# Kernel optimization log

Measured on AMD Instinct MI355X. Metric: run time of the kernel, lower is better.

The kernel has to match this reference:

```python
import jax, jax.numpy as jnp
import numpy as np

N_Q = 16384; N_S = 16384; NN = 32; F_IN = 128; F_OUT = 256
K = 15; DIM = 3
RADIUS = 10.0
KP_EXTENT_CFG = 1.0      # config.NETWORK.KP_EXTENT (also scales learned offsets)
DENSITY = 5.0            # config.NETWORK.DENSITY_PARAMETER
EXTENT = KP_EXTENT_CFG * RADIUS / DENSITY   # 2.0
K_RADIUS = 1.5 * EXTENT
OFFSET_DIM = DIM * (K - 1)  # modulated=False, version=0 -> 42


def setup_inputs() -> dict:
    key = jax.random.key(0)
    ks = jax.random.split(key, 8)
    query_points = jax.random.uniform(ks[0], (N_Q, DIM), dtype=jnp.float32)
    support_points = jax.random.uniform(ks[1], (N_S, DIM), dtype=jnp.float32)
    neighbors = jax.random.randint(ks[2], (N_Q, NN), 0, N_S)
    features = jax.random.normal(ks[3], (N_S, F_IN), dtype=jnp.float32)
    # kernel points: fixed disposition inside ball of radius 1.5*extent, first point at center
    kp = jax.random.normal(ks[4], (K, DIM), dtype=jnp.float32)
    kp = kp / jnp.linalg.norm(kp, axis=1, keepdims=True) * (0.7 * K_RADIUS)
    K_points = kp.at[0].set(0.0)
    weight = jax.random.normal(ks[5], (K, F_IN, F_OUT), dtype=jnp.float32) / np.sqrt(F_IN)
    deformable_weight = jax.random.normal(ks[6], (K, F_IN, OFFSET_DIM), dtype=jnp.float32) / np.sqrt(F_IN)
    bias = jnp.zeros((OFFSET_DIM,), dtype=jnp.float32)
    return {"query_points": query_points, "support_points": support_points,
            "neighbors": neighbors, "features": features, "K_points": K_points,
            "weight": weight, "deformable_weight": deformable_weight, "bias": bias}


def _gather_neighb(query_points, support_points, neighbors, features):
    # pad with shadow point (far away) and zero feature row, as in KPConv_ops
    sp = jnp.concatenate([support_points, jnp.full((1, DIM), 1e6, support_points.dtype)], 0)
    ft = jnp.concatenate([features, jnp.zeros((1, features.shape[1]), features.dtype)], 0)
    rel = sp[neighbors] - query_points[:, None, :]   # [n, nn, 3]
    nfeat = ft[neighbors]                            # [n, nn, f]
    return rel, nfeat


def _linear_influence(sq_dist):
    # KP_INFLUENCE='linear': relu(1 - d/extent); CONVOLUTION_MODE='sum'
    return jnp.maximum(1.0 - jnp.sqrt(sq_dist) / EXTENT, 0.0)


def reference(query_points, support_points, neighbors, features, K_points,
              weight, deformable_weight, bias):
    rel, nfeat = _gather_neighb(query_points, support_points, neighbors, features)

    # --- rigid KPConv producing offsets (version=0) ---
    d0 = rel[:, :, None, :] - K_points[None, None, :, :]   # [n, nn, K, 3]
    sq0 = jnp.sum(d0 * d0, axis=-1)                        # [n, nn, K]
    w0 = _linear_influence(sq0)
    wf0 = jnp.einsum('enk,enf->ekf', w0, nfeat)            # [n, K, f]
    feat0 = jnp.einsum('ekf,kfo->eo', wf0, deformable_weight) + bias  # [n, 42]

    # not modulated: reshape to offsets, prepend zero offset for center kernel point
    offsets = feat0.reshape(-1, K - 1, DIM)
    offsets = jnp.concatenate([jnp.zeros_like(offsets[:, :1, :]), offsets], axis=1)
    offsets = offsets * KP_EXTENT_CFG                      # [n, K, 3]

    # --- deformable KPConv ---
    def_kp = K_points[None, :, :] + offsets                # [n, K, 3]
    d1 = rel[:, :, None, :] - def_kp[:, None, :, :]        # [n, nn, K, 3]
    sq1 = jnp.sum(d1 * d1, axis=-1)                        # [n, nn, K]
    w1 = _linear_influence(sq1)                            # out-of-range neighbors get 0 weight
    wf1 = jnp.einsum('enk,enf->ekf', w1, nfeat)            # [n, K, f]
    out = jnp.einsum('ekf,kfo->eo', wf1, weight)           # [n, f_out]
    return out
```

## Files before the change

### kernel.cpp

```cpp
#include <hip/hip_runtime.h>
#include <hip/hip_bf16.h>
#include <math.h>

typedef __attribute__((ext_vector_type(8))) short bf16x8;
typedef __attribute__((ext_vector_type(4))) float f32x4;

#define NQ 16384
#define NN 32
#define FI 128
#define FO 256
#define KPN 15
#define OD 42
#define INV_EXT 0.5f

#define WS_FP1    0u
#define WS_FP2    (8u * 1024u * 1024u)
#define WS_BSW    (12u * 1024u * 1024u)
#define WS_DWBH   (13u * 1024u * 1024u)
#define WS_DWBL   (WS_DWBH + 196608u)
#define WS_DEFKP  (14u * 1024u * 1024u)

static __device__ __forceinline__ unsigned short f2bf(float x) {
    union { __hip_bfloat16 h; unsigned short u; } cv;
    cv.h = __float2bfloat16(x);
    return cv.u;
}
static __device__ __forceinline__ float bf2f(unsigned short h) {
    union { unsigned int u; float f; } cv;
    cv.u = ((unsigned int)h) << 16;
    return cv.f;
}

union U8 { unsigned short u[8]; bf16x8 v; };

__global__ void pre_all(const float* __restrict__ feat,
                        unsigned int* __restrict__ fp1, unsigned int* __restrict__ fp2,
                        const float* __restrict__ w, unsigned short* __restrict__ Bsw,
                        const float* __restrict__ dw,
                        unsigned short* __restrict__ dhi, unsigned short* __restrict__ dlo)
{
    const int b = blockIdx.x, t = threadIdx.x;
    if (b < 4096) {
        const int tid = b * 256 + t;
        const int s = tid >> 6, r = tid & 63;
        const int fp = r >> 4, low = r & 15;
        const float a = feat[s * FI + fp * 32 + low];
        const float c = feat[s * FI + fp * 32 + 16 + low];
        const unsigned short ha = f2bf(a), hc = f2bf(c);
        const unsigned int w0 = (unsigned int)ha | ((unsigned int)hc << 16);
        const unsigned int w1 = (unsigned int)f2bf(a - bf2f(ha)) |
                                ((unsigned int)f2bf(c - bf2f(hc)) << 16);
        uint2 pr; pr.x = w0; pr.y = w1;
        *(uint2*)&fp1[s * 128 + fp * 32 + low * 2] = pr;
        fp2[s * 64 + fp * 16 + low] = w0;
    } else if (b < 4096 + 256) {
        const int tid = (b - 4096) * 256 + t;
        const int lane = tid & 63;
        const int kt   = (tid >> 6) & 63;
        const int nt   = tid >> 12;
        const int n    = nt * 16 + (lane & 15);
        const int kbase = kt * 32 + (lane >> 4) * 8;
        unsigned int p[4];
        #pragma unroll
        for (int jj = 0; jj < 4; jj++) {
            unsigned int lo, hi;
            {
                const int kk = kbase + 2 * jj;
                const int f = kk >> 4, k = kk & 15;
                lo = (k < KPN) ? f2bf(w[(k * FI + f) * FO + n]) : 0u;
            }
            {
                const int kk = kbase + 2 * jj + 1;
                const int f = kk >> 4, k = kk & 15;
                hi = (k < KPN) ? f2bf(w[(k * FI + f) * FO + n]) : 0u;
            }
            p[jj] = lo | (hi << 16);
        }
        unsigned int* op = (unsigned int*)&Bsw[tid * 8];
        op[0] = p[0]; op[1] = p[1]; op[2] = p[2]; op[3] = p[3];
    } else {
        const int tid = (b - 4352) * 256 + t;
        const int lane = tid & 63;
        const int kt   = (tid >> 6) & 63;
        const int nt   = tid >> 12;
        const int o    = nt * 16 + (lane & 15);
        const int kbase = kt * 32 + (lane >> 4) * 8;
        #pragma unroll
        for (int j = 0; j < 8; j++) {
            const int kf = kbase + j;
            const int f = kf >> 4, k = kf & 15;
            float v = (k < KPN && o < OD) ? dw[(k * FI + f) * OD + o] : 0.f;
            unsigned short h = f2bf(v);
            dhi[tid * 8 + j] = h;
            dlo[tid * 8 + j] = f2bf(v - bf2f(h));
        }
    }
}

__global__ __launch_bounds__(512, 4)
void k1_offsets(const float* __restrict__ query, const float* __restrict__ support,
                const int* __restrict__ neighbors, const unsigned int* __restrict__ fp1,
                const float* __restrict__ kpoints,
                const unsigned short* __restrict__ dwB_hi,
                const unsigned short* __restrict__ dwB_lo,
                const float* __restrict__ bias, float* __restrict__ defkp)
{
    __shared__ unsigned short wfA_hi[8192];
    __shared__ unsigned short wfA_lo[8192];
    __shared__ float relx[512], rely[512], relz[512];
    __shared__ int   nbr_s[512];
    __shared__ float kp_s[48];
    __shared__ f32x4 cred[3 * 64];

    const int t = threadIdx.x;
    const int qbase = blockIdx.x * 16;
    if (t < 45) kp_s[t] = kpoints[t];
    if (t >= 45 && t < 48) kp_s[t] = 0.f;

    {
        const int e = t >> 5, n = t & 31;
        const int q = qbase + e;
        const int idx = neighbors[q * NN + n];
        nbr_s[t] = idx;
        relx[t] = support[idx * 3 + 0] - query[q * 3 + 0];
        rely[t] = support[idx * 3 + 1] - query[q * 3 + 1];
        relz[t] = support[idx * 3 + 2] - query[q * 3 + 2];
    }
    __syncthreads();

    const int wave = t >> 6, lane = t & 63;
    const int quad = lane >> 4, low = lane & 15;
    const int ee0 = wave * 2;

    const int kb = (low < KPN) ? low * 3 : 0;
    const float kx = kp_s[kb + 0], ky = kp_s[kb + 1], kz = kp_s[kb + 2];
    U8 ah[2], al[2];
    #pragma unroll
    for (int ei = 0; ei < 2; ei++) {
        #pragma unroll
        for (int j = 0; j < 8; j++) {
            const int ni = (ee0 + ei) * 32 + quad * 8 + j;
            const float dx = relx[ni] - kx;
            const float dy = rely[ni] - ky;
            const float dz = relz[ni] - kz;
            const float d = sqrtf(dx * dx + dy * dy + dz * dz);
            float w = 1.0f - d * INV_EXT;
            w = (low < KPN && w > 0.f) ? w : 0.f;
            const unsigned short h = f2bf(w);
            ah[ei].u[j] = h;
            al[ei].u[j] = f2bf(w - bf2f(h));
        }
    }

    f32x4 acc = {0.f, 0.f, 0.f, 0.f};
    const int nt = wave >> 1, half = wave & 1;

    for (int c = 0; c < 4; c++) {
        #pragma unroll
        for (int ei = 0; ei < 2; ei++) {
            const int ee = ee0 + ei;
            union { unsigned int u[4]; bf16x8 v; } bhA, blA, bhB, blB;
            #pragma unroll
            for (int jj = 0; jj < 4; jj++) {
                const int r0 = nbr_s[ee * 32 + quad * 8 + 2 * jj];
                const int r1 = nbr_s[ee * 32 + quad * 8 + 2 * jj + 1];
                const uint2 d0 = *(const uint2*)&fp1[r0 * 128 + c * 32 + low * 2];
                const uint2 d1 = *(const uint2*)&fp1[r1 * 128 + c * 32 + low * 2];
                bhA.u[jj] = __builtin_amdgcn_perm(d1.x, d0.x, 0x05040100u);
                bhB.u[jj] = __builtin_amdgcn_perm(d1.x, d0.x, 0x07060302u);
                blA.u[jj] = __builtin_amdgcn_perm(d1.y, d0.y, 0x05040100u);
                blB.u[jj] = __builtin_amdgcn_perm(d1.y, d0.y, 0x07060302u);
            }
            #pragma unroll
            for (int hh2 = 0; hh2 < 2; hh2++) {
                const bf16x8 bh = hh2 ? bhB.v : bhA.v;
                const bf16x8 bl = hh2 ? blB.v : blA.v;
                f32x4 o = {0.f, 0.f, 0.f, 0.f};
                o = __builtin_amdgcn_mfma_f32_16x16x32_bf16(al[ei].v, bh, o, 0, 0, 0);
                o = __builtin_amdgcn_mfma_f32_16x16x32_bf16(ah[ei].v, bl, o, 0, 0, 0);
                o = __builtin_amdgcn_mfma_f32_16x16x32_bf16(ah[ei].v, bh, o, 0, 0, 0);
                const int cblk = (hh2 * 16 + low) * 2 + (quad >> 1);
                const int hw = cblk * 128 + ((ee ^ (cblk & 15)) * 8) + (quad & 1) * 4;
                const unsigned short h0 = f2bf(o[0]), h1 = f2bf(o[1]);
                const unsigned short h2 = f2bf(o[2]), h3 = f2bf(o[3]);
                uint2 ph;
                ph.x = (unsigned int)h0 | ((unsigned int)h1 << 16);
                ph.y = (unsigned int)h2 | ((unsigned int)h3 << 16);
                *(uint2*)&wfA_hi[hw] = ph;
                uint2 pl;
                pl.x = (unsigned int)f2bf(o[0] - bf2f(h0)) |
                       ((unsigned int)f2bf(o[1] - bf2f(h1)) << 16);
                pl.y = (unsigned int)f2bf(o[2] - bf2f(h2)) |
                       ((unsigned int)f2bf(o[3] - bf2f(h3)) << 16);
                *(uint2*)&wfA_lo[hw] = pl;
            }
        }
        __syncthreads();
        if (wave < 6) {
            const bf16x8* Bh = (const bf16x8*)dwB_hi;
            const bf16x8* Bl = (const bf16x8*)dwB_lo;
            #pragma unroll 4
            for (int ktl = half * 8; ktl < half * 8 + 8; ktl++) {
                const int cblk = ktl * 4 + quad;
                const int hw = cblk * 128 + ((low ^ (cblk & 15)) * 8);
                bf16x8 a_h = *(const bf16x8*)&wfA_hi[hw];
                bf16x8 a_l = *(const bf16x8*)&wfA_lo[hw];
                const int ktg = c * 16 + ktl;
                bf16x8 b_h = Bh[(nt * 64 + ktg) * 64 + lane];
                bf16x8 b_l = Bl[(nt * 64 + ktg) * 64 + lane];
                acc = __builtin_amdgcn_mfma_f32_16x16x32_bf16(a_l, b_h, acc, 0, 0, 0);
                acc = __builtin_amdgcn_mfma_f32_16x16x32_bf16(a_h, b_l, acc, 0, 0, 0);
                acc = __builtin_amdgcn_mfma_f32_16x16x32_bf16(a_h, b_h, acc, 0, 0, 0);
            }
        } else if (c == 0 && wave == 6 && lane < 48) {
            defkp[(qbase + lane / 3) * 45 + (lane % 3)] = kp_s[lane % 3];
        }
        __syncthreads();
    }

    if (wave < 6 && half == 1) cred[nt * 64 + lane] = acc;
    __syncthreads();
    if (wave < 6 && half == 0) {
        f32x4 o2 = cred[nt * 64 + lane];
        acc[0] += o2[0]; acc[1] += o2[1]; acc[2] += o2[2]; acc[3] += o2[3];
        const int o = nt * 16 + low;
        if (o < OD) {
            const float bo = bias[o] + kp_s[3 + o];
            #pragma unroll
            for (int r = 0; r < 4; r++) {
                const int ee = quad * 4 + r;
                defkp[(qbase + ee) * 45 + 3 + o] = bo + acc[r];
            }
        }
    }
}

__global__ __launch_bounds__(512, 4)
void k2_deform(const float* __restrict__ query, const float* __restrict__ support,
               const int* __restrict__ neighbors, const unsigned int* __restrict__ fp2,
               const unsigned short* __restrict__ Bsw, const float* __restrict__ defkp,
               float* __restrict__ out)
{
    __shared__ unsigned short wfA[16384];
    __shared__ float relx[1024], rely[1024], relz[1024];
    __shared__ float dk_s[32 * 45];
    __shared__ unsigned short nbr_s[1024];

    const int t = threadIdx.x;
    const int qbase = blockIdx.x * 32;

    for (int i = t; i < 32 * 45; i += 512) dk_s[i] = defkp[qbase * 45 + i];
    #pragma unroll
    for (int ii = 0; ii < 2; ii++) {
        const int i = ii * 512 + t;
        const int e = i >> 5, n = i & 31;
        const int q = qbase + e;
        const int idx = neighbors[q * NN + n];
        nbr_s[i] = (unsigned short)idx;
        relx[i] = support[idx * 3 + 0] - query[q * 3 + 0];
        rely[i] = support[idx * 3 + 1] - query[q * 3 + 1];
        relz[i] = support[idx * 3 + 2] - query[q * 3 + 2];
    }
    __syncthreads();

    const int wave = t >> 6, lane = t & 63;
    const int quad = lane >> 4, low = lane & 15;
    const int ee0 = wave * 4;
    const int kb = (low < KPN) ? low * 3 : 0;

    U8 af[4];
    #pragma unroll
    for (int ei = 0; ei < 4; ei++) {
        const int ee = ee0 + ei;
        const float kx = dk_s[ee * 45 + kb + 0];
        const float ky = dk_s[ee * 45 + kb + 1];
        const float kz = dk_s[ee * 45 + kb + 2];
        #pragma unroll
        for (int j = 0; j < 8; j++) {
            const int ni = ee * 32 + quad * 8 + j;
            const float dx = relx[ni] - kx;
            const float dy = rely[ni] - ky;
            const float dz = relz[ni] - kz;
            const float d = sqrtf(dx * dx + dy * dy + dz * dz);
            float w = 1.0f - d * INV_EXT;
            w = (low < KPN && w > 0.f) ? w : 0.f;
            af[ei].u[j] = f2bf(w);
        }
    }

    f32x4 acc00 = {0,0,0,0}, acc01 = {0,0,0,0};
    f32x4 acc10 = {0,0,0,0}, acc11 = {0,0,0,0};
    const int nt0 = wave * 2, nt1 = nt0 + 1;
    const bf16x8* Bp = (const bf16x8*)Bsw;

    for (int c = 0; c < 4; c++) {
        #pragma unroll
        for (int ei = 0; ei < 4; ei++) {
            const int ee = ee0 + ei;
            union { unsigned int u[4]; bf16x8 v; } bA, bB;
            #pragma unroll
            for (int jj = 0; jj < 4; jj++) {
                const int r0 = nbr_s[ee * 32 + quad * 8 + 2 * jj];
                const int r1 = nbr_s[ee * 32 + quad * 8 + 2 * jj + 1];
                const unsigned int d0 = fp2[r0 * 64 + c * 16 + low];
                const unsigned int d1 = fp2[r1 * 64 + c * 16 + low];
                bA.u[jj] = __builtin_amdgcn_perm(d1, d0, 0x05040100u);
                bB.u[jj] = __builtin_amdgcn_perm(d1, d0, 0x07060302u);
            }
            #pragma unroll
            for (int hh2 = 0; hh2 < 2; hh2++) {
                const bf16x8 b = hh2 ? bB.v : bA.v;
                f32x4 o = {0.f, 0.f, 0.f, 0.f};
                o = __builtin_amdgcn_mfma_f32_16x16x32_bf16(af[ei].v, b, o, 0, 0, 0);
                const int cblk = (hh2 * 16 + low) * 2 + (quad >> 1);
                const int hw = cblk * 256 + ((ee ^ (cblk & 31)) * 8) + (quad & 1) * 4;
                uint2 ph;
                ph.x = (unsigned int)f2bf(o[0]) | ((unsigned int)f2bf(o[1]) << 16);
                ph.y = (unsigned int)f2bf(o[2]) | ((unsigned int)f2bf(o[3]) << 16);
                *(uint2*)&wfA[hw] = ph;
            }
        }
        __syncthreads();
        #pragma unroll 4
        for (int ktl = 0; ktl < 16; ktl++) {
            const int cblk = ktl * 4 + quad;
            const int s0 = (low ^ (cblk & 31)) * 8;
            const int s1 = ((16 + low) ^ (cblk & 31)) * 8;
            bf16x8 a0 = *(const bf16x8*)&wfA[cblk * 256 + s0];
            bf16x8 a1 = *(const bf16x8*)&wfA[cblk * 256 + s1];
            const int ktg = c * 16 + ktl;
            bf16x8 b0 = Bp[(nt0 * 64 + ktg) * 64 + lane];
            bf16x8 b1 = Bp[(nt1 * 64 + ktg) * 64 + lane];
            acc00 = __builtin_amdgcn_mfma_f32_16x16x32_bf16(a0, b0, acc00, 0, 0, 0);
            acc01 = __builtin_amdgcn_mfma_f32_16x16x32_bf16(a0, b1, acc01, 0, 0, 0);
            acc10 = __builtin_amdgcn_mfma_f32_16x16x32_bf16(a1, b0, acc10, 0, 0, 0);
            acc11 = __builtin_amdgcn_mfma_f32_16x16x32_bf16(a1, b1, acc11, 0, 0, 0);
        }
        __syncthreads();
    }

    #pragma unroll
    for (int r = 0; r < 4; r++) {
        const int e0 = quad * 4 + r;
        out[(qbase + e0) * FO + nt0 * 16 + low] = acc00[r];
        out[(qbase + e0) * FO + nt1 * 16 + low] = acc01[r];
        out[(qbase + 16 + e0) * FO + nt0 * 16 + low] = acc10[r];
        out[(qbase + 16 + e0) * FO + nt1 * 16 + low] = acc11[r];
    }
}

extern "C" void kernel_launch(void* const* d_in, const int* in_sizes, int n_in,
                              void* d_out, int out_size, void* d_ws, size_t ws_size,
                              hipStream_t stream) {
    const float* query     = (const float*)d_in[0];
    const float* support   = (const float*)d_in[1];
    const int*   neighbors = (const int*)  d_in[2];
    const float* features  = (const float*)d_in[3];
    const float* kpoints   = (const float*)d_in[4];
    const float* weight    = (const float*)d_in[5];
    const float* dweight   = (const float*)d_in[6];
    const float* bias      = (const float*)d_in[7];
    float*       out       = (float*)d_out;

    char* ws = (char*)d_ws;
    unsigned int*   fp1  = (unsigned int*)(ws + WS_FP1);
    unsigned int*   fp2  = (unsigned int*)(ws + WS_FP2);
    unsigned short* Bsw  = (unsigned short*)(ws + WS_BSW);
    unsigned short* dwBh = (unsigned short*)(ws + WS_DWBH);
    unsigned short* dwBl = (unsigned short*)(ws + WS_DWBL);
    float*          defkp = (float*)(ws + WS_DEFKP);

    pre_all<<<4400, 256, 0, stream>>>(features, fp1, fp2, weight, Bsw,
                                      dweight, dwBh, dwBl);
    k1_offsets<<<NQ / 16, 512, 0, stream>>>(query, support, neighbors, fp1,
                                            kpoints, dwBh, dwBl, bias, defkp);
    k2_deform<<<NQ / 32, 512, 0, stream>>>(query, support, neighbors, fp2,
                                           Bsw, defkp, out);
}
```

Baseline: 167.7 us.

## Fuse offset KPConv and deformable KPConv into one kernel per 32 queries

Merges the offset-producing kernel and the deformable convolution kernel into a single kernel handling 32 queries per block. The deformed kernel points stay in shared memory instead of going through a global buffer, and the neighbor and relative-position setup is shared between both stages. The offset GEMM is re-tiled so that 6 waves each cover one of 3 output tiles for one of two 16-query halves, which removes the cross-wave reduction. The cost is higher shared memory per block (two 32 KB feature tiles plus position arrays), which may lower occupancy, and half as many blocks for the offset stage.

```diff
diff --git a/kernel.cpp b/kernel.cpp
--- a/kernel.cpp
+++ b/kernel.cpp
@@ -18,7 +18,6 @@
 #define WS_BSW    (12u * 1024u * 1024u)
 #define WS_DWBH   (13u * 1024u * 1024u)
 #define WS_DWBL   (WS_DWBH + 196608u)
-#define WS_DEFKP  (14u * 1024u * 1024u)
 
 static __device__ __forceinline__ unsigned short f2bf(float x) {
     union { __hip_bfloat16 h; unsigned short u; } cv;
@@ -98,158 +97,25 @@
 }
 
 __global__ __launch_bounds__(512, 4)
-void k1_offsets(const float* __restrict__ query, const float* __restrict__ support,
-                const int* __restrict__ neighbors, const unsigned int* __restrict__ fp1,
-                const float* __restrict__ kpoints,
-                const unsigned short* __restrict__ dwB_hi,
-                const unsigned short* __restrict__ dwB_lo,
-                const float* __restrict__ bias, float* __restrict__ defkp)
+void k_fused(const float* __restrict__ query, const float* __restrict__ support,
+             const int* __restrict__ neighbors, const unsigned int* __restrict__ fp1,
+             const unsigned int* __restrict__ fp2, const float* __restrict__ kpoints,
+             const unsigned short* __restrict__ dwB_hi,
+             const unsigned short* __restrict__ dwB_lo,
+             const unsigned short* __restrict__ Bsw,
+             const float* __restrict__ bias, float* __restrict__ out)
 {
-    __shared__ unsigned short wfA_hi[8192];
-    __shared__ unsigned short wfA_lo[8192];
-    __shared__ float relx[512], rely[512], relz[512];
-    __shared__ int   nbr_s[512];
+    __shared__ unsigned short wf_hi[16384];
+    __shared__ unsigned short wf_lo[16384];
+    __shared__ float relx[1024], rely[1024], relz[1024];
+    __shared__ unsigned short nbr_s[1024];
     __shared__ float kp_s[48];
-    __shared__ f32x4 cred[3 * 64];
 
     const int t = threadIdx.x;
-    const int qbase = blockIdx.x * 16;
+    const int qbase = blockIdx.x * 32;
     if (t < 45) kp_s[t] = kpoints[t];
     if (t >= 45 && t < 48) kp_s[t] = 0.f;
 
-    {
-        const int e = t >> 5, n = t & 31;
-        const int q = qbase + e;
-        const int idx = neighbors[q * NN + n];
-        nbr_s[t] = idx;
-        relx[t] = support[idx * 3 + 0] - query[q * 3 + 0];
-        rely[t] = support[idx * 3 + 1] - query[q * 3 + 1];
-        relz[t] = support[idx * 3 + 2] - query[q * 3 + 2];
-    }
-    __syncthreads();
-
-    const int wave = t >> 6, lane = t & 63;
-    const int quad = lane >> 4, low = lane & 15;
-    const int ee0 = wave * 2;
-
-    const int kb = (low < KPN) ? low * 3 : 0;
-    const float kx = kp_s[kb + 0], ky = kp_s[kb + 1], kz = kp_s[kb + 2];
-    U8 ah[2], al[2];
-    #pragma unroll
-    for (int ei = 0; ei < 2; ei++) {
-        #pragma unroll
-        for (int j = 0; j < 8; j++) {
-            const int ni = (ee0 + ei) * 32 + quad * 8 + j;
-            const float dx = relx[ni] - kx;
-            const float dy = rely[ni] - ky;
-            const float dz = relz[ni] - kz;
-            const float d = sqrtf(dx * dx + dy * dy + dz * dz);
-            float w = 1.0f - d * INV_EXT;
-            w = (low < KPN && w > 0.f) ? w : 0.f;
-            const unsigned short h = f2bf(w);
-            ah[ei].u[j] = h;
-            al[ei].u[j] = f2bf(w - bf2f(h));
-        }
-    }
-
-    f32x4 acc = {0.f, 0.f, 0.f, 0.f};
-    const int nt = wave >> 1, half = wave & 1;
-
-    for (int c = 0; c < 4; c++) {
-        #pragma unroll
-        for (int ei = 0; ei < 2; ei++) {
-            const int ee = ee0 + ei;
-            union { unsigned int u[4]; bf16x8 v; } bhA, blA, bhB, blB;
-            #pragma unroll
-            for (int jj = 0; jj < 4; jj++) {
-                const int r0 = nbr_s[ee * 32 + quad * 8 + 2 * jj];
-                const int r1 = nbr_s[ee * 32 + quad * 8 + 2 * jj + 1];
-                const uint2 d0 = *(const uint2*)&fp1[r0 * 128 + c * 32 + low * 2];
-                const uint2 d1 = *(const uint2*)&fp1[r1 * 128 + c * 32 + low * 2];
-                bhA.u[jj] = __builtin_amdgcn_perm(d1.x, d0.x, 0x05040100u);
-                bhB.u[jj] = __builtin_amdgcn_perm(d1.x, d0.x, 0x07060302u);
-                blA.u[jj] = __builtin_amdgcn_perm(d1.y, d0.y, 0x05040100u);
-                blB.u[jj] = __builtin_amdgcn_perm(d1.y, d0.y, 0x07060302u);
-            }
-            #pragma unroll
-            for (int hh2 = 0; hh2 < 2; hh2++) {
-                const bf16x8 bh = hh2 ? bhB.v : bhA.v;
-                const bf16x8 bl = hh2 ? blB.v : blA.v;
-                f32x4 o = {0.f, 0.f, 0.f, 0.f};
-                o = __builtin_amdgcn_mfma_f32_16x16x32_bf16(al[ei].v, bh, o, 0, 0, 0);
-                o = __builtin_amdgcn_mfma_f32_16x16x32_bf16(ah[ei].v, bl, o, 0, 0, 0);
-                o = __builtin_amdgcn_mfma_f32_16x16x32_bf16(ah[ei].v, bh, o, 0, 0, 0);
-                const int cblk = (hh2 * 16 + low) * 2 + (quad >> 1);
-                const int hw = cblk * 128 + ((ee ^ (cblk & 15)) * 8) + (quad & 1) * 4;
-                const unsigned short h0 = f2bf(o[0]), h1 = f2bf(o[1]);
-                const unsigned short h2 = f2bf(o[2]), h3 = f2bf(o[3]);
-                uint2 ph;
-                ph.x = (unsigned int)h0 | ((unsigned int)h1 << 16);
-                ph.y = (unsigned int)h2 | ((unsigned int)h3 << 16);
-                *(uint2*)&wfA_hi[hw] = ph;
-                uint2 pl;
-                pl.x = (unsigned int)f2bf(o[0] - bf2f(h0)) |
-                       ((unsigned int)f2bf(o[1] - bf2f(h1)) << 16);
-                pl.y = (unsigned int)f2bf(o[2] - bf2f(h2)) |
-                       ((unsigned int)f2bf(o[3] - bf2f(h3)) << 16);
-                *(uint2*)&wfA_lo[hw] = pl;
-            }
-        }
-        __syncthreads();
-        if (wave < 6) {
-            const bf16x8* Bh = (const bf16x8*)dwB_hi;
-            const bf16x8* Bl = (const bf16x8*)dwB_lo;
-            #pragma unroll 4
-            for (int ktl = half * 8; ktl < half * 8 + 8; ktl++) {
-                const int cblk = ktl * 4 + quad;
-                const int hw = cblk * 128 + ((low ^ (cblk & 15)) * 8);
-                bf16x8 a_h = *(const bf16x8*)&wfA_hi[hw];
-                bf16x8 a_l = *(const bf16x8*)&wfA_lo[hw];
-                const int ktg = c * 16 + ktl;
-                bf16x8 b_h = Bh[(nt * 64 + ktg) * 64 + lane];
-                bf16x8 b_l = Bl[(nt * 64 + ktg) * 64 + lane];
-                acc = __builtin_amdgcn_mfma_f32_16x16x32_bf16(a_l, b_h, acc, 0, 0, 0);
-                acc = __builtin_amdgcn_mfma_f32_16x16x32_bf16(a_h, b_l, acc, 0, 0, 0);
-                acc = __builtin_amdgcn_mfma_f32_16x16x32_bf16(a_h, b_h, acc, 0, 0, 0);
-            }
-        } else if (c == 0 && wave == 6 && lane < 48) {
-            defkp[(qbase + lane / 3) * 45 + (lane % 3)] = kp_s[lane % 3];
-        }
-        __syncthreads();
-    }
-
-    if (wave < 6 && half == 1) cred[nt * 64 + lane] = acc;
-    __syncthreads();
-    if (wave < 6 && half == 0) {
-        f32x4 o2 = cred[nt * 64 + lane];
-        acc[0] += o2[0]; acc[1] += o2[1]; acc[2] += o2[2]; acc[3] += o2[3];
-        const int o = nt * 16 + low;
-        if (o < OD) {
-            const float bo = bias[o] + kp_s[3 + o];
-            #pragma unroll
-            for (int r = 0; r < 4; r++) {
-                const int ee = quad * 4 + r;
-                defkp[(qbase + ee) * 45 + 3 + o] = bo + acc[r];
-            }
-        }
-    }
-}
-
-__global__ __launch_bounds__(512, 4)
-void k2_deform(const float* __restrict__ query, const float* __restrict__ support,
-               const int* __restrict__ neighbors, const unsigned int* __restrict__ fp2,
-               const unsigned short* __restrict__ Bsw, const float* __restrict__ defkp,
-               float* __restrict__ out)
-{
-    __shared__ unsigned short wfA[16384];
-    __shared__ float relx[1024], rely[1024], relz[1024];
-    __shared__ float dk_s[32 * 45];
-    __shared__ unsigned short nbr_s[1024];
-
-    const int t = threadIdx.x;
-    const int qbase = blockIdx.x * 32;
-
-    for (int i = t; i < 32 * 45; i += 512) dk_s[i] = defkp[qbase * 45 + i];
     #pragma unroll
     for (int ii = 0; ii < 2; ii++) {
         const int i = ii * 512 + t;
@@ -265,16 +131,122 @@
 
     const int wave = t >> 6, lane = t & 63;
     const int quad = lane >> 4, low = lane & 15;
-    const int ee0 = wave * 4;
     const int kb = (low < KPN) ? low * 3 : 0;
+
+    U8 ah[4], al[4];
+    {
+        const float kx = kp_s[kb + 0], ky = kp_s[kb + 1], kz = kp_s[kb + 2];
+        #pragma unroll
+        for (int ei = 0; ei < 4; ei++) {
+            const int ee = wave * 4 + ei;
+            #pragma unroll
+            for (int j = 0; j < 8; j++) {
+                const int ni = ee * 32 + quad * 8 + j;
+                const float dx = relx[ni] - kx;
+                const float dy = rely[ni] - ky;
+                const float dz = relz[ni] - kz;
+                const float d = sqrtf(dx * dx + dy * dy + dz * dz);
+                float w = 1.0f - d * INV_EXT;
+                w = (low < KPN && w > 0.f) ? w : 0.f;
+                const unsigned short h = f2bf(w);
+                ah[ei].u[j] = h;
+                al[ei].u[j] = f2bf(w - bf2f(h));
+            }
+        }
+    }
+
+    f32x4 acc = {0.f, 0.f, 0.f, 0.f};
+    const int et = (wave >= 3) ? 1 : 0;
+    const int nt = wave - et * 3;
+
+    for (int c = 0; c < 4; c++) {
+        #pragma unroll 2
+        for (int ei = 0; ei < 4; ei++) {
+            const int ee = wave * 4 + ei;
+            union { unsigned int u[4]; bf16x8 v; } bhA, blA, bhB, blB;
+            #pragma unroll
+            for (int jj = 0; jj < 4; jj++) {
+                const int r0 = nbr_s[ee * 32 + quad * 8 + 2 * jj];
+                const int r1 = nbr_s[ee * 32 + quad * 8 + 2 * jj + 1];
+                const uint2 d0 = *(const uint2*)&fp1[r0 * 128 + c * 32 + low * 2];
+                const uint2 d1 = *(const uint2*)&fp1[r1 * 128 + c * 32 + low * 2];
+                bhA.u[jj] = __builtin_amdgcn_perm(d1.x, d0.x, 0x05040100u);
+                bhB.u[jj] = __builtin_amdgcn_perm(d1.x, d0.x, 0x07060302u);
+                blA.u[jj] = __builtin_amdgcn_perm(d1.y, d0.y, 0x05040100u);
+                blB.u[jj] = __builtin_amdgcn_perm(d1.y, d0.y, 0x07060302u);
+            }
+            #pragma unroll
+            for (int hh2 = 0; hh2 < 2; hh2++) {
+                const bf16x8 bh = hh2 ? bhB.v : bhA.v;
+                const bf16x8 bl = hh2 ? blB.v : blA.v;
+                f32x4 o = {0.f, 0.f, 0.f, 0.f};
+                o = __builtin_amdgcn_mfma_f32_16x16x32_bf16(al[ei].v, bh, o, 0, 0, 0);
+                o = __builtin_amdgcn_mfma_f32_16x16x32_bf16(ah[ei].v, bl, o, 0, 0, 0);
+                o = __builtin_amdgcn_mfma_f32_16x16x32_bf16(ah[ei].v, bh, o, 0, 0, 0);
+                const int fc   = hh2 * 16 + low;
+                const int cblk = fc + (quad >> 1) * 32;
+                const int slot = ee ^ fc;
+                const int hw   = cblk * 256 + slot * 8 + (quad & 1) * 4;
+                const unsigned short h0 = f2bf(o[0]), h1 = f2bf(o[1]);
+                const unsigned short h2 = f2bf(o[2]), h3 = f2bf(o[3]);
+                uint2 ph;
+                ph.x = (unsigned int)h0 | ((unsigned int)h1 << 16);
+                ph.y = (unsigned int)h2 | ((unsigned int)h3 << 16);
+                *(uint2*)&wf_hi[hw] = ph;
+                uint2 pl;
+                pl.x = (unsigned int)f2bf(o[0] - bf2f(h0)) |
+                       ((unsigned int)f2bf(o[1] - bf2f(h1)) << 16);
+                pl.y = (unsigned int)f2bf(o[2] - bf2f(h2)) |
+                       ((unsigned int)f2bf(o[3] - bf2f(h3)) << 16);
+                *(uint2*)&wf_lo[hw] = pl;
+            }
+        }
+        __syncthreads();
+        if (wave < 6) {
+            const bf16x8* Bh = (const bf16x8*)dwB_hi;
+            const bf16x8* Bl = (const bf16x8*)dwB_lo;
+            #pragma unroll 4
+            for (int ktl = 0; ktl < 16; ktl++) {
+                const int fcq  = ktl * 2 + (quad >> 1);
+                const int cblk = fcq + (quad & 1) * 32;
+                const int slot = (et * 16 + low) ^ fcq;
+                bf16x8 a_h = *(const bf16x8*)&wf_hi[cblk * 256 + slot * 8];
+                bf16x8 a_l = *(const bf16x8*)&wf_lo[cblk * 256 + slot * 8];
+                const int ktg = c * 16 + ktl;
+                bf16x8 b_h = Bh[(nt * 64 + ktg) * 64 + lane];
+                bf16x8 b_l = Bl[(nt * 64 + ktg) * 64 + lane];
+                acc = __builtin_amdgcn_mfma_f32_16x16x32_bf16(a_l, b_h, acc, 0, 0, 0);
+                acc = __builtin_amdgcn_mfma_f32_16x16x32_bf16(a_h, b_l, acc, 0, 0, 0);
+                acc = __builtin_amdgcn_mfma_f32_16x16x32_bf16(a_h, b_h, acc, 0, 0, 0);
+            }
+        }
+        __syncthreads();
+    }
+
+    float* dk_s = (float*)wf_lo;
+    if (wave < 6) {
+        const int o = nt * 16 + low;
+        if (o < OD) {
+            const float bo = bias[o] + kp_s[3 + o];
+            #pragma unroll
+            for (int r = 0; r < 4; r++) {
+                const int ee = et * 16 + quad * 4 + r;
+                dk_s[ee * 48 + 3 + o] = bo + acc[r];
+            }
+        }
+    } else {
+        const int idx2 = (wave - 6) * 64 + lane;
+        if (idx2 < 96) dk_s[(idx2 / 3) * 48 + (idx2 % 3)] = kp_s[idx2 % 3];
+    }
+    __syncthreads();
 
     U8 af[4];
     #pragma unroll
     for (int ei = 0; ei < 4; ei++) {
-        const int ee = ee0 + ei;
-        const float kx = dk_s[ee * 45 + kb + 0];
-        const float ky = dk_s[ee * 45 + kb + 1];
-        const float kz = dk_s[ee * 45 + kb + 2];
+        const int ee = wave * 4 + ei;
+        const float kx = dk_s[ee * 48 + kb + 0];
+        const float ky = dk_s[ee * 48 + kb + 1];
+        const float kz = dk_s[ee * 48 + kb + 2];
         #pragma unroll
         for (int j = 0; j < 8; j++) {
             const int ni = ee * 32 + quad * 8 + j;
@@ -296,7 +268,7 @@
     for (int c = 0; c < 4; c++) {
         #pragma unroll
         for (int ei = 0; ei < 4; ei++) {
-            const int ee = ee0 + ei;
+            const int ee = wave * 4 + ei;
             union { unsigned int u[4]; bf16x8 v; } bA, bB;
             #pragma unroll
             for (int jj = 0; jj < 4; jj++) {
@@ -312,22 +284,25 @@
                 const bf16x8 b = hh2 ? bB.v : bA.v;
                 f32x4 o = {0.f, 0.f, 0.f, 0.f};
                 o = __builtin_amdgcn_mfma_f32_16x16x32_bf16(af[ei].v, b, o, 0, 0, 0);
-                const int cblk = (hh2 * 16 + low) * 2 + (quad >> 1);
-                const int hw = cblk * 256 + ((ee ^ (cblk & 31)) * 8) + (quad & 1) * 4;
+                const int fc   = hh2 * 16 + low;
+                const int cblk = fc + (quad >> 1) * 32;
+                const int slot = ee ^ fc;
+                const int hw   = cblk * 256 + slot * 8 + (quad & 1) * 4;
                 uint2 ph;
                 ph.x = (unsigned int)f2bf(o[0]) | ((unsigned int)f2bf(o[1]) << 16);
                 ph.y = (unsigned int)f2bf(o[2]) | ((unsigned int)f2bf(o[3]) << 16);
-                *(uint2*)&wfA[hw] = ph;
+                *(uint2*)&wf_hi[hw] = ph;
             }
         }
         __syncthreads();
         #pragma unroll 4
         for (int ktl = 0; ktl < 16; ktl++) {
-            const int cblk = ktl * 4 + quad;
-            const int s0 = (low ^ (cblk & 31)) * 8;
-            const int s1 = ((16 + low) ^ (cblk & 31)) * 8;
-            bf16x8 a0 = *(const bf16x8*)&wfA[cblk * 256 + s0];
-            bf16x8 a1 = *(const bf16x8*)&wfA[cblk * 256 + s1];
+            const int fcq  = ktl * 2 + (quad >> 1);
+            const int cblk = fcq + (quad & 1) * 32;
+            const int s0 = (low ^ fcq) * 8;
+            const int s1 = ((16 + low) ^ fcq) * 8;
+            bf16x8 a0 = *(const bf16x8*)&wf_hi[cblk * 256 + s0];
+            bf16x8 a1 = *(const bf16x8*)&wf_hi[cblk * 256 + s1];
             const int ktg = c * 16 + ktl;
             bf16x8 b0 = Bp[(nt0 * 64 + ktg) * 64 + lane];
             bf16x8 b1 = Bp[(nt1 * 64 + ktg) * 64 + lane];
@@ -368,12 +343,9 @@
     unsigned short* Bsw  = (unsigned short*)(ws + WS_BSW);
     unsigned short* dwBh = (unsigned short*)(ws + WS_DWBH);
     unsigned short* dwBl = (unsigned short*)(ws + WS_DWBL);
-    float*          defkp = (float*)(ws + WS_DEFKP);
 
     pre_all<<<4400, 256, 0, stream>>>(features, fp1, fp2, weight, Bsw,
                                       dweight, dwBh, dwBl);
-    k1_offsets<<<NQ / 16, 512, 0, stream>>>(query, support, neighbors, fp1,
-                                            kpoints, dwBh, dwBl, bias, defkp);
-    k2_deform<<<NQ / 32, 512, 0, stream>>>(query, support, neighbors, fp2,
-                                           Bsw, defkp, out);
-}
+    k_fused<<<NQ / 32, 512, 0, stream>>>(query, support, neighbors, fp1, fp2,
+                                         kpoints, dwBh, dwBl, Bsw, bias, out);
+}
```

Result: slower. 178.6 us (+6.5%).

## Vectorize feature packing and widen k2 gathers to two feature chunks per pass

Applied to the files above, without the earlier changes.

The feature pre-pack now uses float4 loads and uint4 stores, with four times fewer blocks, and lays out fp2 so one uint2 gather covers two 32-feature chunks. k2 then processes two chunks per LDS staging pass, halving the chunk-loop barrier count. It reuses a single 64KB LDS buffer that aliases the rel/dk scratch arrays, with an added barrier. k1's LDS swizzle layout for the staged wf tile is also changed. The larger LDS footprint in k2 may reduce occupancy.

```diff
diff --git a/kernel.cpp b/kernel.cpp
--- a/kernel.cpp
+++ b/kernel.cpp
@@ -40,21 +40,31 @@
                         unsigned short* __restrict__ dhi, unsigned short* __restrict__ dlo)
 {
     const int b = blockIdx.x, t = threadIdx.x;
-    if (b < 4096) {
-        const int tid = b * 256 + t;
-        const int s = tid >> 6, r = tid & 63;
-        const int fp = r >> 4, low = r & 15;
-        const float a = feat[s * FI + fp * 32 + low];
-        const float c = feat[s * FI + fp * 32 + 16 + low];
-        const unsigned short ha = f2bf(a), hc = f2bf(c);
-        const unsigned int w0 = (unsigned int)ha | ((unsigned int)hc << 16);
-        const unsigned int w1 = (unsigned int)f2bf(a - bf2f(ha)) |
-                                ((unsigned int)f2bf(c - bf2f(hc)) << 16);
-        uint2 pr; pr.x = w0; pr.y = w1;
-        *(uint2*)&fp1[s * 128 + fp * 32 + low * 2] = pr;
-        fp2[s * 64 + fp * 16 + low] = w0;
-    } else if (b < 4096 + 256) {
-        const int tid = (b - 4096) * 256 + t;
+    if (b < 1024) {
+        const int g  = b * 256 + t;
+        const int lq = g & 3;
+        const int fp = (g >> 2) & 3;
+        const int s  = g >> 4;
+        const float4* f4 = (const float4*)feat;
+        const float4 A = f4[s * 32 + fp * 8 + lq];
+        const float4 C = f4[s * 32 + fp * 8 + 4 + lq];
+        const float av[4] = {A.x, A.y, A.z, A.w};
+        const float cv[4] = {C.x, C.y, C.z, C.w};
+        unsigned int pw[8];
+        #pragma unroll
+        for (int e = 0; e < 4; e++) {
+            const unsigned short ha = f2bf(av[e]), hc = f2bf(cv[e]);
+            const unsigned short la = f2bf(av[e] - bf2f(ha));
+            const unsigned short lc = f2bf(cv[e] - bf2f(hc));
+            pw[2 * e]     = (unsigned int)ha | ((unsigned int)hc << 16);
+            pw[2 * e + 1] = (unsigned int)la | ((unsigned int)lc << 16);
+            fp2[s * 64 + (fp >> 1) * 32 + (lq * 4 + e) * 2 + (fp & 1)] =
+                (unsigned int)ha | ((unsigned int)hc << 16);
+        }
+        *(uint4*)&fp1[s * 128 + fp * 32 + lq * 8]     = *(uint4*)&pw[0];
+        *(uint4*)&fp1[s * 128 + fp * 32 + lq * 8 + 4] = *(uint4*)&pw[4];
+    } else if (b < 1024 + 256) {
+        const int tid = (b - 1024) * 256 + t;
         const int lane = tid & 63;
         const int kt   = (tid >> 6) & 63;
         const int nt   = tid >> 12;
@@ -79,7 +89,7 @@
         unsigned int* op = (unsigned int*)&Bsw[tid * 8];
         op[0] = p[0]; op[1] = p[1]; op[2] = p[2]; op[3] = p[3];
     } else {
-        const int tid = (b - 4352) * 256 + t;
+        const int tid = (b - 1280) * 256 + t;
         const int lane = tid & 63;
         const int kt   = (tid >> 6) & 63;
         const int nt   = tid >> 12;
@@ -105,8 +115,8 @@
                 const unsigned short* __restrict__ dwB_lo,
                 const float* __restrict__ bias, float* __restrict__ defkp)
 {
-    __shared__ unsigned short wfA_hi[8192];
-    __shared__ unsigned short wfA_lo[8192];
+    __shared__ unsigned short wf_hi[8192];
+    __shared__ unsigned short wf_lo[8192];
     __shared__ float relx[512], rely[512], relz[512];
     __shared__ int   nbr_s[512];
     __shared__ float kp_s[48];
@@ -130,42 +140,47 @@
 
     const int wave = t >> 6, lane = t & 63;
     const int quad = lane >> 4, low = lane & 15;
-    const int ee0 = wave * 2;
-
     const int kb = (low < KPN) ? low * 3 : 0;
-    const float kx = kp_s[kb + 0], ky = kp_s[kb + 1], kz = kp_s[kb + 2];
+
     U8 ah[2], al[2];
-    #pragma unroll
-    for (int ei = 0; ei < 2; ei++) {
-        #pragma unroll
-        for (int j = 0; j < 8; j++) {
-            const int ni = (ee0 + ei) * 32 + quad * 8 + j;
-            const float dx = relx[ni] - kx;
-            const float dy = rely[ni] - ky;
-            const float dz = relz[ni] - kz;
-            const float d = sqrtf(dx * dx + dy * dy + dz * dz);
-            float w = 1.0f - d * INV_EXT;
-            w = (low < KPN && w > 0.f) ? w : 0.f;
-            const unsigned short h = f2bf(w);
-            ah[ei].u[j] = h;
-            al[ei].u[j] = f2bf(w - bf2f(h));
+    {
+        const float kx = kp_s[kb + 0], ky = kp_s[kb + 1], kz = kp_s[kb + 2];
+        #pragma unroll
+        for (int ei = 0; ei < 2; ei++) {
+            const int ee = wave * 2 + ei;
+            #pragma unroll
+            for (int j = 0; j < 8; j++) {
+                const int ni = ee * 32 + quad * 8 + j;
+                const float dx = relx[ni] - kx;
+                const float dy = rely[ni] - ky;
+                const float dz = relz[ni] - kz;
+                const float d = sqrtf(dx * dx + dy * dy + dz * dz);
+                float w = 1.0f - d * INV_EXT;
+                w = (low < KPN && w > 0.f) ? w : 0.f;
+                const unsigned short h = f2bf(w);
+                ah[ei].u[j] = h;
+                al[ei].u[j] = f2bf(w - bf2f(h));
+            }
         }
     }
 
     f32x4 acc = {0.f, 0.f, 0.f, 0.f};
     const int nt = wave >> 1, half = wave & 1;
+    const uint2* fp1v = (const uint2*)fp1;
+    const bf16x8* Bh = (const bf16x8*)dwB_hi;
+    const bf16x8* Bl = (const bf16x8*)dwB_lo;
 
     for (int c = 0; c < 4; c++) {
         #pragma unroll
         for (int ei = 0; ei < 2; ei++) {
-            const int ee = ee0 + ei;
+            const int ee = wave * 2 + ei;
             union { unsigned int u[4]; bf16x8 v; } bhA, blA, bhB, blB;
             #pragma unroll
             for (int jj = 0; jj < 4; jj++) {
                 const int r0 = nbr_s[ee * 32 + quad * 8 + 2 * jj];
                 const int r1 = nbr_s[ee * 32 + quad * 8 + 2 * jj + 1];
-                const uint2 d0 = *(const uint2*)&fp1[r0 * 128 + c * 32 + low * 2];
-                const uint2 d1 = *(const uint2*)&fp1[r1 * 128 + c * 32 + low * 2];
+                const uint2 d0 = fp1v[r0 * 64 + c * 16 + low];
+                const uint2 d1 = fp1v[r1 * 64 + c * 16 + low];
                 bhA.u[jj] = __builtin_amdgcn_perm(d1.x, d0.x, 0x05040100u);
                 bhB.u[jj] = __builtin_amdgcn_perm(d1.x, d0.x, 0x07060302u);
                 blA.u[jj] = __builtin_amdgcn_perm(d1.y, d0.y, 0x05040100u);
@@ -179,32 +194,34 @@
                 o = __builtin_amdgcn_mfma_f32_16x16x32_bf16(al[ei].v, bh, o, 0, 0, 0);
                 o = __builtin_amdgcn_mfma_f32_16x16x32_bf16(ah[ei].v, bl, o, 0, 0, 0);
                 o = __builtin_amdgcn_mfma_f32_16x16x32_bf16(ah[ei].v, bh, o, 0, 0, 0);
-                const int cblk = (hh2 * 16 + low) * 2 + (quad >> 1);
-                const int hw = cblk * 128 + ((ee ^ (cblk & 15)) * 8) + (quad & 1) * 4;
+                const int fc   = hh2 * 16 + low;
+                const int cblk = fc + (quad >> 1) * 32;
+                const int slot = ee ^ (fc & 15);
+                const int hw   = cblk * 128 + slot * 8 + (quad & 1) * 4;
                 const unsigned short h0 = f2bf(o[0]), h1 = f2bf(o[1]);
                 const unsigned short h2 = f2bf(o[2]), h3 = f2bf(o[3]);
                 uint2 ph;
                 ph.x = (unsigned int)h0 | ((unsigned int)h1 << 16);
                 ph.y = (unsigned int)h2 | ((unsigned int)h3 << 16);
-                *(uint2*)&wfA_hi[hw] = ph;
+                *(uint2*)&wf_hi[hw] = ph;
                 uint2 pl;
                 pl.x = (unsigned int)f2bf(o[0] - bf2f(h0)) |
                        ((unsigned int)f2bf(o[1] - bf2f(h1)) << 16);
                 pl.y = (unsigned int)f2bf(o[2] - bf2f(h2)) |
                        ((unsigned int)f2bf(o[3] - bf2f(h3)) << 16);
-                *(uint2*)&wfA_lo[hw] = pl;
+                *(uint2*)&wf_lo[hw] = pl;
             }
         }
         __syncthreads();
         if (wave < 6) {
-            const bf16x8* Bh = (const bf16x8*)dwB_hi;
-            const bf16x8* Bl = (const bf16x8*)dwB_lo;
             #pragma unroll 4
             for (int ktl = half * 8; ktl < half * 8 + 8; ktl++) {
-                const int cblk = ktl * 4 + quad;
-                const int hw = cblk * 128 + ((low ^ (cblk & 15)) * 8);
-                bf16x8 a_h = *(const bf16x8*)&wfA_hi[hw];
-                bf16x8 a_l = *(const bf16x8*)&wfA_lo[hw];
+                const int fc   = ktl * 2 + (quad >> 1);
+                const int cblk = fc + (quad & 1) * 32;
+                const int slot = low ^ (fc & 15);
+                const int hw   = cblk * 128 + slot * 8;
+                bf16x8 a_h = *(const bf16x8*)&wf_hi[hw];
+                bf16x8 a_l = *(const bf16x8*)&wf_lo[hw];
                 const int ktg = c * 16 + ktl;
                 bf16x8 b_h = Bh[(nt * 64 + ktg) * 64 + lane];
                 bf16x8 b_l = Bl[(nt * 64 + ktg) * 64 + lane];
@@ -241,10 +258,13 @@
                const unsigned short* __restrict__ Bsw, const float* __restrict__ defkp,
                float* __restrict__ out)
 {
-    __shared__ unsigned short wfA[16384];
-    __shared__ float relx[1024], rely[1024], relz[1024];
-    __shared__ float dk_s[32 * 45];
+    __shared__ unsigned short wf2[32768];
     __shared__ unsigned short nbr_s[1024];
+
+    float* relx = (float*)wf2;
+    float* rely = relx + 1024;
+    float* relz = relx + 2048;
+    float* dk_s = relx + 3072;
 
     const int t = threadIdx.x;
     const int qbase = blockIdx.x * 32;
@@ -265,13 +285,12 @@
 
     const int wave = t >> 6, lane = t & 63;
     const int quad = lane >> 4, low = lane & 15;
-    const int ee0 = wave * 4;
     const int kb = (low < KPN) ? low * 3 : 0;
 
     U8 af[4];
     #pragma unroll
     for (int ei = 0; ei < 4; ei++) {
-        const int ee = ee0 + ei;
+        const int ee = wave * 4 + ei;
         const float kx = dk_s[ee * 45 + kb + 0];
         const float ky = dk_s[ee * 45 + kb + 1];
         const float kz = dk_s[ee * 45 + kb + 2];
@@ -287,54 +306,68 @@
             af[ei].u[j] = f2bf(w);
         }
     }
+    __syncthreads();
 
     f32x4 acc00 = {0,0,0,0}, acc01 = {0,0,0,0};
     f32x4 acc10 = {0,0,0,0}, acc11 = {0,0,0,0};
     const int nt0 = wave * 2, nt1 = nt0 + 1;
     const bf16x8* Bp = (const bf16x8*)Bsw;
-
-    for (int c = 0; c < 4; c++) {
+    const uint2* fp2v = (const uint2*)fp2;
+
+    for (int c2 = 0; c2 < 2; c2++) {
         #pragma unroll
         for (int ei = 0; ei < 4; ei++) {
-            const int ee = ee0 + ei;
-            union { unsigned int u[4]; bf16x8 v; } bA, bB;
+            const int ee = wave * 4 + ei;
+            union { unsigned int u[4]; bf16x8 v; } b00, b01, b10, b11;
             #pragma unroll
             for (int jj = 0; jj < 4; jj++) {
                 const int r0 = nbr_s[ee * 32 + quad * 8 + 2 * jj];
                 const int r1 = nbr_s[ee * 32 + quad * 8 + 2 * jj + 1];
-                const unsigned int d0 = fp2[r0 * 64 + c * 16 + low];
-                const unsigned int d1 = fp2[r1 * 64 + c * 16 + low];
-                bA.u[jj] = __builtin_amdgcn_perm(d1, d0, 0x05040100u);
-                bB.u[jj] = __builtin_amdgcn_perm(d1, d0, 0x07060302u);
-            }
-            #pragma unroll
-            for (int hh2 = 0; hh2 < 2; hh2++) {
-                const bf16x8 b = hh2 ? bB.v : bA.v;
-                f32x4 o = {0.f, 0.f, 0.f, 0.f};
-                o = __builtin_amdgcn_mfma_f32_16x16x32_bf16(af[ei].v, b, o, 0, 0, 0);
-                const int cblk = (hh2 * 16 + low) * 2 + (quad >> 1);
-                const int hw = cblk * 256 + ((ee ^ (cblk & 31)) * 8) + (quad & 1) * 4;
-                uint2 ph;
-                ph.x = (unsigned int)f2bf(o[0]) | ((unsigned int)f2bf(o[1]) << 16);
-                ph.y = (unsigned int)f2bf(o[2]) | ((unsigned int)f2bf(o[3]) << 16);
-                *(uint2*)&wfA[hw] = ph;
+                const uint2 g0 = fp2v[r0 * 32 + c2 * 16 + low];
+                const uint2 g1 = fp2v[r1 * 32 + c2 * 16 + low];
+                b00.u[jj] = __builtin_amdgcn_perm(g1.x, g0.x, 0x05040100u);
+                b01.u[jj] = __builtin_amdgcn_perm(g1.x, g0.x, 0x07060302u);
+                b10.u[jj] = __builtin_amdgcn_perm(g1.y, g0.y, 0x05040100u);
+                b11.u[jj] = __builtin_amdgcn_perm(g1.y, g0.y, 0x07060302u);
+            }
+            #pragma unroll
+            for (int p = 0; p < 2; p++) {
+                #pragma unroll
+                for (int hh2 = 0; hh2 < 2; hh2++) {
+                    const bf16x8 b = p ? (hh2 ? b11.v : b10.v)
+                                       : (hh2 ? b01.v : b00.v);
+                    f32x4 o = {0.f, 0.f, 0.f, 0.f};
+                    o = __builtin_amdgcn_mfma_f32_16x16x32_bf16(af[ei].v, b, o, 0, 0, 0);
+                    const int fc   = hh2 * 16 + low;
+                    const int cblk = fc + (quad >> 1) * 32;
+                    const int slot = ee ^ fc;
+                    const int hw   = p * 16384 + cblk * 256 + slot * 8 + (quad & 1) * 4;
+                    uint2 ph;
+                    ph.x = (unsigned int)f2bf(o[0]) | ((unsigned int)f2bf(o[1]) << 16);
+                    ph.y = (unsigned int)f2bf(o[2]) | ((unsigned int)f2bf(o[3]) << 16);
+                    *(uint2*)&wf2[hw] = ph;
+                }
             }
         }
         __syncthreads();
-        #pragma unroll 4
-        for (int ktl = 0; ktl < 16; ktl++) {
-            const int cblk = ktl * 4 + quad;
-            const int s0 = (low ^ (cblk & 31)) * 8;
-            const int s1 = ((16 + low) ^ (cblk & 31)) * 8;
-            bf16x8 a0 = *(const bf16x8*)&wfA[cblk * 256 + s0];
-            bf16x8 a1 = *(const bf16x8*)&wfA[cblk * 256 + s1];
-            const int ktg = c * 16 + ktl;
-            bf16x8 b0 = Bp[(nt0 * 64 + ktg) * 64 + lane];
-            bf16x8 b1 = Bp[(nt1 * 64 + ktg) * 64 + lane];
-            acc00 = __builtin_amdgcn_mfma_f32_16x16x32_bf16(a0, b0, acc00, 0, 0, 0);
-            acc01 = __builtin_amdgcn_mfma_f32_16x16x32_bf16(a0, b1, acc01, 0, 0, 0);
-            acc10 = __builtin_amdgcn_mfma_f32_16x16x32_bf16(a1, b0, acc10, 0, 0, 0);
-            acc11 = __builtin_amdgcn_mfma_f32_16x16x32_bf16(a1, b1, acc11, 0, 0, 0);
+        #pragma unroll
+        for (int p = 0; p < 2; p++) {
+            #pragma unroll 4
+            for (int ktl = 0; ktl < 16; ktl++) {
+                const int fc   = ktl * 2 + (quad >> 1);
+                const int cblk = fc + (quad & 1) * 32;
+                const int s0 = (low ^ fc) * 8;
+                const int s1 = ((16 + low) ^ fc) * 8;
+                bf16x8 a0 = *(const bf16x8*)&wf2[p * 16384 + cblk * 256 + s0];
+                bf16x8 a1 = *(const bf16x8*)&wf2[p * 16384 + cblk * 256 + s1];
+                const int ktg = (2 * c2 + p) * 16 + ktl;
+                bf16x8 b0 = Bp[(nt0 * 64 + ktg) * 64 + lane];
+                bf16x8 b1 = Bp[(nt1 * 64 + ktg) * 64 + lane];
+                acc00 = __builtin_amdgcn_mfma_f32_16x16x32_bf16(a0, b0, acc00, 0, 0, 0);
+                acc01 = __builtin_amdgcn_mfma_f32_16x16x32_bf16(a0, b1, acc01, 0, 0, 0);
+                acc10 = __builtin_amdgcn_mfma_f32_16x16x32_bf16(a1, b0, acc10, 0, 0, 0);
+                acc11 = __builtin_amdgcn_mfma_f32_16x16x32_bf16(a1, b1, acc11, 0, 0, 0);
+            }
         }
         __syncthreads();
     }
@@ -370,7 +403,7 @@
     unsigned short* dwBl = (unsigned short*)(ws + WS_DWBL);
     float*          defkp = (float*)(ws + WS_DEFKP);
 
-    pre_all<<<4400, 256, 0, stream>>>(features, fp1, fp2, weight, Bsw,
+    pre_all<<<1328, 256, 0, stream>>>(features, fp1, fp2, weight, Bsw,
                                       dweight, dwBh, dwBl);
     k1_offsets<<<NQ / 16, 512, 0, stream>>>(query, support, neighbors, fp1,
                                             kpoints, dwBh, dwBl, bias, defkp);
```

Measured after the change: 165.2 us. About the same (-1.5%).
